# Kernel optimization log

Hardware: AMD Instinct MI355X
Metric: run time of the kernel (lower is better)

## Reference

```python
import jax, jax.numpy as jnp
import numpy as np

B, CIN, H, W = 32, 16, 64, 64
COUT, K, STRIDE = 32, 3, 1


def setup_inputs() -> dict:
    key = jax.random.key(0)
    k1, k2, k3 = jax.random.split(key, 3)
    x = jax.random.normal(k1, (B, CIN, H, W), dtype=jnp.float32)
    # per-location kernels (Ho, Wo, Cout, Cin, K, K); kaiming-ish scale
    fan_in = CIN * K * K
    bound = float(np.sqrt(3.0 / fan_in))
    weights = jax.random.uniform(k2, (H, W, COUT, CIN, K, K), dtype=jnp.float32,
                                 minval=-bound, maxval=bound)
    bias = jax.random.normal(k3, (H, W, COUT), dtype=jnp.float32)
    return {"x": x, "weights": weights, "bias": bias}


def reference(x, weights, bias):
    Ho, Wo, co, ci, k, _ = weights.shape
    pad = k // 2
    if k % 2 == 1:
        padding = [(pad, pad), (pad, pad)]
    else:
        padding = [(pad - 1, pad), (pad - 1, pad)]
    # im2col: (B, ci*k*k, Ho, Wo); feature dim ordered channel-slowest, matching
    # torch's (C, k, k) flatten after unfold+permute.
    patches = jax.lax.conv_general_dilated_patches(
        x, (k, k), (STRIDE, STRIDE), padding)
    w = weights.reshape(Ho, Wo, co, ci * k * k)
    # per-location matmul: out[b,o,h,w] = sum_p patches[b,p,h,w] * w[h,w,o,p]
    out = jnp.einsum('bphw,hwop->bohw', patches, w)
    out = out + bias.transpose(2, 0, 1)[None]  # (1, Cout, Ho, Wo)
    return out
```

## Files before the change

kernel.cpp:

```cpp
#include <hip/hip_runtime.h>


#define CIN  16
#define HW_  4096
#define PP   144
#define RST  20
#define BST  962

typedef float v4f  __attribute__((ext_vector_type(4)));
typedef float v16f __attribute__((ext_vector_type(16)));
typedef short v8s  __attribute__((ext_vector_type(8)));

__device__ __forceinline__ unsigned short f2bf(float f) {
    unsigned int u = __builtin_bit_cast(unsigned int, f);
    u += 0x7fffu + ((u >> 16) & 1u);
    return (unsigned short)(u >> 16);
}
__device__ __forceinline__ unsigned int pk2(float a, float b) {
    return (unsigned int)f2bf(a) | ((unsigned int)f2bf(b) << 16);
}
__device__ __forceinline__ constexpr int offp(int p) {
    const int c = p / 9, rem = p % 9, r = rem / 3, kw = rem % 3;
    return (c * 3 + r) * RST + kw + 1;
}

__global__ __launch_bounds__(1024, 4) void xonv_kernel(
    const float* __restrict__ x,
    const float* __restrict__ wt,
    const float* __restrict__ bias,
    float* __restrict__ out)
{
    const int t  = threadIdx.x;
    const int bi = blockIdx.x;
    const int h  = ((bi >> 5) << 3) + (bi & 7);
    const int wg = (bi >> 3) & 3;
    const int w0 = wg << 4;

    __shared__ unsigned short xs[32 * BST];
    float* ol = (float*)xs;

    const int l  = t & 63;
    const int wv = t >> 6;
    const int w  = w0 + wv;
    const int o  = l & 31;
    const int kh = l >> 5;

    const float* wp = wt + (size_t)(h * 64 + w) * (32 * PP)
                         + (size_t)o * PP + kh * 8;
    float4 ca[4], cb[4];
#pragma unroll
    for (int s = 0; s < 4; ++s) {
        ca[s] = *(const float4*)(wp + s * 16);
        cb[s] = *(const float4*)(wp + s * 16 + 4);
    }
    const float bia = bias[(size_t)(h * 64 + w) * 32 + o];

    const int wstart = w0 - 4;
#pragma unroll
    for (int i = 0; i < 9; ++i) {
        const int j   = t + i * 1024;
        const int rid = (int)(((unsigned)j * 43691u) >> 18);
        const int sub = j - rid * 6;
        const int b   = (rid * 683) >> 15;
        const int cr  = rid - b * 48;
        const int c   = (cr * 43) >> 7;
        const int r   = cr - c * 3;
        const int row = h + r - 1;
        const int col4 = wstart + sub * 4;
        float4 f = {0.f, 0.f, 0.f, 0.f};
        if ((unsigned)row < 64u && (unsigned)col4 <= 60u)
            f = *(const float4*)(x + ((size_t)(b * CIN + c)) * HW_
                                   + row * 64 + col4);
        unsigned short* dst = xs + b * BST + cr * RST;
        if (sub == 0) {
            ((unsigned int*)dst)[0] = pk2(f.z, f.w);
        } else if (sub == 5) {
            ((unsigned int*)dst)[9] = pk2(f.x, f.y);
        } else {
            unsigned int* d = (unsigned int*)(dst + sub * 4 - 2);
            d[0] = pk2(f.x, f.y);
            d[1] = pk2(f.z, f.w);
        }
    }
    __syncthreads();

    const int gb = o * BST + wv;

    v16f acc;
#pragma unroll
    for (int i = 0; i < 16; ++i) acc[i] = 0.f;

#pragma unroll
    for (int kc = 0; kc < 9; ++kc) {
        const int slot = kc & 3;

        union { unsigned int u[4]; v8s s; } ub;
        ub.u[0] = pk2(ca[slot].x, ca[slot].y);
        ub.u[1] = pk2(ca[slot].z, ca[slot].w);
        ub.u[2] = pk2(cb[slot].x, cb[slot].y);
        ub.u[3] = pk2(cb[slot].z, cb[slot].w);

        if (kc + 4 < 9) {
            ca[slot] = *(const float4*)(wp + (kc + 4) * 16);
            cb[slot] = *(const float4*)(wp + (kc + 4) * 16 + 4);
        }

        v8s a;
#pragma unroll
        for (int j = 0; j < 8; ++j) {
            const int C0 = offp(kc * 16 + j);
            const int C1 = offp(kc * 16 + 8 + j);
            a[j] = (short)xs[gb + (kh ? C1 : C0)];
        }

        acc = __builtin_amdgcn_mfma_f32_32x32x16_bf16(a, ub.s, acc, 0, 0, 0);
    }

    __syncthreads();

#pragma unroll
    for (int half = 0; half < 2; ++half) {
#pragma unroll
        for (int rr = 0; rr < 8; ++rr) {
            const int r     = half * 8 + rr;
            const int browl = (r & 3) + 8 * ((r >> 2) & 1) + 4 * kh;
            ol[(browl * 32 + o) * 17 + wv] = acc[r] + bia;
        }
        __syncthreads();
#pragma unroll
        for (int i2 = 0; i2 < 2; ++i2) {
            const int flat = t + i2 * 1024;
            const int bol  = flat >> 2;
            const int q4   = flat & 3;
            const int base = bol * 17 + q4 * 4;
            float4 v;
            v.x = ol[base + 0]; v.y = ol[base + 1];
            v.z = ol[base + 2]; v.w = ol[base + 3];
            const int bg = half * 16 + (bol >> 5);
            const int og = bol & 31;
            *(float4*)(out + ((size_t)(bg * 32 + og)) * HW_
                           + h * 64 + w0 + q4 * 4) = v;
        }
        __syncthreads();
    }
}

extern "C" void kernel_launch(void* const* d_in, const int* in_sizes, int n_in,
                              void* d_out, int out_size, void* d_ws, size_t ws_size,
                              hipStream_t stream) {
    const float* x       = (const float*)d_in[0];
    const float* weights = (const float*)d_in[1];
    const float* bias    = (const float*)d_in[2];
    float* out           = (float*)d_out;
    (void)in_sizes; (void)n_in; (void)out_size; (void)d_ws; (void)ws_size;

    dim3 grid(256);
    dim3 block(1024);
    hipLaunchKernelGGL(xonv_kernel, grid, block, 0, stream, x, weights, bias, out);
}
```

Before: 124.3 us.

## Stage per-location weights through double-buffered LDS with block-cooperative loads

Instead of each wave loading its own location's weights with strided per-lane float4 reads, all 1024 threads cooperatively load one location's contiguous 4608-float weight slab per phase, convert to bf16 and store it into a double-buffered LDS tile. Only one wave computes each phase while the others prefetch, which serializes the 16 waves' MFMA work across 16 barrier-separated phases. The aim is fully coalesced global weight reads. The cost is 16 block-wide syncs, extra LDS traffic, and idle compute in all but one wave per phase.

```diff
diff --git a/kernel.cpp b/kernel.cpp
--- a/kernel.cpp
+++ b/kernel.cpp
@@ -6,6 +6,9 @@
 #define PP   144
 #define RST  20
 #define BST  962
+#define LOCF 4608
+#define WPAD 152
+#define WBUF 4864
 
 typedef float v4f  __attribute__((ext_vector_type(4)));
 typedef float v16f __attribute__((ext_vector_type(16)));
@@ -37,6 +40,7 @@
     const int w0 = wg << 4;
 
     __shared__ unsigned short xs[32 * BST];
+    __shared__ unsigned short wlds[2 * WBUF];
     float* ol = (float*)xs;
 
     const int l  = t & 63;
@@ -45,14 +49,23 @@
     const int o  = l & 31;
     const int kh = l >> 5;
 
-    const float* wp = wt + (size_t)(h * 64 + w) * (32 * PP)
-                         + (size_t)o * PP + kh * 8;
-    float4 ca[4], cb[4];
-#pragma unroll
-    for (int s = 0; s < 4; ++s) {
-        ca[s] = *(const float4*)(wp + s * 16);
-        cb[s] = *(const float4*)(wp + s * 16 + 4);
-    }
+    const int q0  = t;
+    const int o0  = (q0 * 1821) >> 16;
+    const int r0  = q0 - o0 * 36;
+    const int q1  = t + 1024;
+    const int o1  = (q1 * 1821) >> 16;
+    const int r1  = q1 - o1 * 36;
+    const bool j2 = (t < 128);
+
+    const float* wbase = wt + (size_t)(h * 64 + w0) * LOCF;
+
+    v4f a0A = *(const v4f*)(wbase + 0 * LOCF + q0 * 4);
+    v4f a1A = {0.f, 0.f, 0.f, 0.f};
+    if (j2) a1A = *(const v4f*)(wbase + 0 * LOCF + q1 * 4);
+    v4f a0B = *(const v4f*)(wbase + 1 * LOCF + q0 * 4);
+    v4f a1B = {0.f, 0.f, 0.f, 0.f};
+    if (j2) a1B = *(const v4f*)(wbase + 1 * LOCF + q1 * 4);
+
     const float bia = bias[(size_t)(h * 64 + w) * 32 + o];
 
     const int wstart = w0 - 4;
@@ -82,6 +95,16 @@
             d[1] = pk2(f.z, f.w);
         }
     }
+
+    {
+        unsigned int* wb = (unsigned int*)wlds;
+        wb[o0 * 76 + r0 * 2]     = pk2(a0A.x, a0A.y);
+        wb[o0 * 76 + r0 * 2 + 1] = pk2(a0A.z, a0A.w);
+        if (j2) {
+            wb[o1 * 76 + r1 * 2]     = pk2(a1A.x, a1A.y);
+            wb[o1 * 76 + r1 * 2 + 1] = pk2(a1A.z, a1A.w);
+        }
+    }
     __syncthreads();
 
     const int gb = o * BST + wv;
@@ -90,33 +113,58 @@
 #pragma unroll
     for (int i = 0; i < 16; ++i) acc[i] = 0.f;
 
-#pragma unroll
-    for (int kc = 0; kc < 9; ++kc) {
-        const int slot = kc & 3;
-
-        union { unsigned int u[4]; v8s s; } ub;
-        ub.u[0] = pk2(ca[slot].x, ca[slot].y);
-        ub.u[1] = pk2(ca[slot].z, ca[slot].w);
-        ub.u[2] = pk2(cb[slot].x, cb[slot].y);
-        ub.u[3] = pk2(cb[slot].z, cb[slot].w);
-
-        if (kc + 4 < 9) {
-            ca[slot] = *(const float4*)(wp + (kc + 4) * 16);
-            cb[slot] = *(const float4*)(wp + (kc + 4) * 16 + 4);
-        }
-
-        v8s a;
-#pragma unroll
-        for (int j = 0; j < 8; ++j) {
-            const int C0 = offp(kc * 16 + j);
-            const int C1 = offp(kc * 16 + 8 + j);
-            a[j] = (short)xs[gb + (kh ? C1 : C0)];
-        }
-
-        acc = __builtin_amdgcn_mfma_f32_32x32x16_bf16(a, ub.s, acc, 0, 0, 0);
-    }
-
-    __syncthreads();
+#define PHASE(J, RA0, RA1, RB0, RB1)                                           \
+    {                                                                          \
+        if ((J) + 2 < 16) {                                                    \
+            RA0 = *(const v4f*)(wbase + ((J) + 2) * LOCF + q0 * 4);            \
+            if (j2) RA1 = *(const v4f*)(wbase + ((J) + 2) * LOCF + q1 * 4);    \
+        }                                                                      \
+        if ((J) + 1 < 16) {                                                    \
+            unsigned int* wb = (unsigned int*)&wlds[(((J) + 1) & 1) * WBUF];   \
+            wb[o0 * 76 + r0 * 2]     = pk2(RB0.x, RB0.y);                      \
+            wb[o0 * 76 + r0 * 2 + 1] = pk2(RB0.z, RB0.w);                      \
+            if (j2) {                                                          \
+                wb[o1 * 76 + r1 * 2]     = pk2(RB1.x, RB1.y);                  \
+                wb[o1 * 76 + r1 * 2 + 1] = pk2(RB1.z, RB1.w);                  \
+            }                                                                  \
+        }                                                                      \
+        if (wv == (J)) {                                                       \
+            const unsigned short* wfr =                                        \
+                &wlds[((J) & 1) * WBUF + o * WPAD + kh * 8];                   \
+            _Pragma("unroll")                                                  \
+            for (int kc = 0; kc < 9; ++kc) {                                   \
+                v8s bs = *(const v8s*)(wfr + kc * 16);                         \
+                v8s a;                                                         \
+                _Pragma("unroll")                                              \
+                for (int jj = 0; jj < 8; ++jj) {                               \
+                    const int C0 = offp(kc * 16 + jj);                         \
+                    const int C1 = offp(kc * 16 + 8 + jj);                     \
+                    a[jj] = (short)xs[gb + (kh ? C1 : C0)];                    \
+                }                                                              \
+                acc = __builtin_amdgcn_mfma_f32_32x32x16_bf16(a, bs, acc,      \
+                                                              0, 0, 0);        \
+            }                                                                  \
+        }                                                                      \
+        __syncthreads();                                                       \
+    }
+
+    PHASE(0,  a0A, a1A, a0B, a1B)
+    PHASE(1,  a0B, a1B, a0A, a1A)
+    PHASE(2,  a0A, a1A, a0B, a1B)
+    PHASE(3,  a0B, a1B, a0A, a1A)
+    PHASE(4,  a0A, a1A, a0B, a1B)
+    PHASE(5,  a0B, a1B, a0A, a1A)
+    PHASE(6,  a0A, a1A, a0B, a1B)
+    PHASE(7,  a0B, a1B, a0A, a1A)
+    PHASE(8,  a0A, a1A, a0B, a1B)
+    PHASE(9,  a0B, a1B, a0A, a1A)
+    PHASE(10, a0A, a1A, a0B, a1B)
+    PHASE(11, a0B, a1B, a0A, a1A)
+    PHASE(12, a0A, a1A, a0B, a1B)
+    PHASE(13, a0B, a1B, a0A, a1A)
+    PHASE(14, a0A, a1A, a0B, a1B)
+    PHASE(15, a0B, a1B, a0A, a1A)
+#undef PHASE
 
 #pragma unroll
     for (int half = 0; half < 2; ++half) {
```

Measured after the change: 130.7 us. 1.05x slower.
